# Performance work log

Measured on AMD Instinct MI355X. Metric: run time of the kernel, lower is better.

Reference implementation:

```python
import jax, jax.numpy as jnp
import numpy as np

N = 200000   # nodes
E = 600000   # edges
D = 128      # input_channels
H = 128      # hidden_channels
EPS = 1e-5   # BatchNorm1d eps


def setup_inputs() -> dict:
    key = jax.random.key(0)
    ks = jax.random.split(key, 6)
    x = jax.random.normal(ks[0], (N, D), dtype=jnp.float32)
    edge_index = jax.random.randint(ks[1], (2, E), 0, N)
    a1 = jnp.full((1,), 0.25, dtype=jnp.float32)   # PReLU init
    gamma = jnp.ones((D,), dtype=jnp.float32)
    beta = jnp.zeros((D,), dtype=jnp.float32)
    W1 = jax.random.normal(ks[2], (D, H), dtype=jnp.float32) / np.float32(np.sqrt(D))
    b1 = jnp.zeros((H,), dtype=jnp.float32)
    a2 = jnp.full((1,), 0.25, dtype=jnp.float32)
    W2 = jax.random.normal(ks[3], (H, D), dtype=jnp.float32) / np.float32(np.sqrt(H))
    b2 = jnp.zeros((D,), dtype=jnp.float32)
    return dict(x=x, edge_index=edge_index, a1=a1, gamma=gamma, beta=beta,
                W1=W1, b1=b1, a2=a2, W2=W2, b2=b2)


def _prelu(x, a):
    return jnp.where(x >= 0, x, a[0] * x)


def _batchnorm(x, gamma, beta):
    # training-mode BatchNorm1d: batch mean, biased variance
    mean = jnp.mean(x, axis=0)
    var = jnp.mean(jnp.square(x - mean), axis=0)
    return (x - mean) * jax.lax.rsqrt(var + EPS) * gamma + beta


def _gcn_conv(x, W, b, src, dst, n):
    # PyG GCNConv: add self-loops, symmetric normalization D^-1/2 (A+I) D^-1/2
    h = x @ W                                            # [n, out]
    deg = jnp.ones((n,), h.dtype).at[dst].add(1.0)       # degree incl. self-loop
    dinv = jax.lax.rsqrt(deg)
    coef = (dinv[src] * dinv[dst])[:, None]              # [E, 1]
    msg = h[src] * coef                                  # gather  [E, out]
    out = jax.ops.segment_sum(msg, dst, num_segments=n)  # scatter [n, out]
    out = out + h * (1.0 / deg)[:, None]                 # self-loop term
    return out + b


def reference(x, edge_index, a1, gamma, beta, W1, b1, a2, W2, b2):
    src, dst = edge_index[0], edge_index[1]
    n = x.shape[0]
    h = _prelu(x, a1)
    h = _batchnorm(h, gamma, beta)
    h = _gcn_conv(h, W1, b1, src, dst, n)
    h = _prelu(h, a2)
    h = _gcn_conv(h, W2, b2, src, dst, n)
    return h
```

## Files before the change

### kernel.cpp

```cpp
#include <hip/hip_runtime.h>

#define NN 200000
#define NE 600000
#define DD 128
#define GT 1563

constexpr float BN_EPS = 1e-5f;

typedef unsigned short u16;
typedef short bf16x8 __attribute__((ext_vector_type(8)));
typedef float f32x4  __attribute__((ext_vector_type(4)));


__global__ void k_zero(int* __restrict__ cnt, float* __restrict__ ssum, float* __restrict__ ssq) {
  int i = blockIdx.x*256 + threadIdx.x;
  if (i < NN) cnt[i] = 0;
  if (i < DD) { ssum[i] = 0.f; ssq[i] = 0.f; }
}

__global__ void k_count(const int* __restrict__ ei, int* __restrict__ cnt) {
  int e = blockIdx.x*256 + threadIdx.x;
  if (e < NE) atomicAdd(&cnt[ei[NE + e]], 1);
}

__global__ void k_stats(const float* __restrict__ x, const float* __restrict__ a1p,
                        float* __restrict__ ssum, float* __restrict__ ssq) {
  __shared__ float s1[8][128], s2[8][128];
  const int c4 = (threadIdx.x & 31) * 4;
  const int rg = threadIdx.x >> 5;
  float a1 = *a1p;
  float acc1[4] = {0.f,0.f,0.f,0.f}, acc2[4] = {0.f,0.f,0.f,0.f};
  const int stride = gridDim.x * 8;
  for (int r = blockIdx.x*8 + rg; r < NN; r += stride) {
    float4 v = *(const float4*)(x + (size_t)r*DD + c4);
    float vv[4] = {v.x, v.y, v.z, v.w};
    #pragma unroll
    for (int i = 0; i < 4; ++i) {
      float u = vv[i];
      u = (u >= 0.f) ? u : a1*u;
      acc1[i] += u; acc2[i] += u*u;
    }
  }
  *(float4*)&s1[rg][c4] = make_float4(acc1[0], acc1[1], acc1[2], acc1[3]);
  *(float4*)&s2[rg][c4] = make_float4(acc2[0], acc2[1], acc2[2], acc2[3]);
  __syncthreads();
  if (threadIdx.x < 128) {
    int col = threadIdx.x;
    float t1 = 0.f, t2 = 0.f;
    #pragma unroll
    for (int g = 0; g < 8; ++g) { t1 += s1[g][col]; t2 += s2[g][col]; }
    atomicAdd(&ssum[col], t1);
    atomicAdd(&ssq [col], t2);
  }
}

__global__ void k_bn_tw1(const float* __restrict__ ssum, const float* __restrict__ ssq,
                         const float* __restrict__ gamma, const float* __restrict__ beta,
                         const float* __restrict__ W1,
                         float* __restrict__ sarr, float* __restrict__ tarr,
                         float* __restrict__ tw1) {
  __shared__ float ts[128];
  int j = threadIdx.x;
  float mean = ssum[j] * (1.f/NN);
  float var  = ssq[j] * (1.f/NN) - mean*mean;
  float s = gamma[j] * rsqrtf(var + BN_EPS);
  float t = beta[j] - mean*s;
  sarr[j] = s; tarr[j] = t; ts[j] = t;
  __syncthreads();
  float acc = 0.f;
  #pragma unroll 8
  for (int k = 0; k < 128; ++k) acc += ts[k] * W1[k*DD + j];
  tw1[j] = acc;
}

__global__ void k_wprep(const float* __restrict__ W, const float* __restrict__ s,
                        u16* __restrict__ hi, u16* __restrict__ lo) {
  int idx = blockIdx.x*256 + threadIdx.x;
  int j = idx >> 7, k = idx & 127;
  float v = W[(size_t)k*DD + j];
  if (s) v *= s[k];
  unsigned hb = __float_as_uint(v) & 0xffff0000u;
  float r = v - __uint_as_float(hb);
  hi[idx] = (u16)(hb >> 16);
  lo[idx] = (u16)(__float_as_uint(r) >> 16);
}


__global__ void k_scan1(const int* __restrict__ cnt, int* __restrict__ rp, int* __restrict__ bsums) {
  __shared__ int sm[256];
  int tid = threadIdx.x;
  int base = blockIdx.x*1024 + tid*4;
  int4 v = make_int4(0,0,0,0);
  if (base + 3 < NN) v = *(const int4*)(cnt + base);
  else {
    if (base   < NN) v.x = cnt[base];
    if (base+1 < NN) v.y = cnt[base+1];
    if (base+2 < NN) v.z = cnt[base+2];
    if (base+3 < NN) v.w = cnt[base+3];
  }
  int p1 = v.x, p2 = p1 + v.y, p3 = p2 + v.z, tsum = p3 + v.w;
  sm[tid] = tsum; __syncthreads();
  for (int off = 1; off < 256; off <<= 1) {
    int t = (tid >= off) ? sm[tid - off] : 0; __syncthreads();
    sm[tid] += t; __syncthreads();
  }
  int inc = sm[tid];
  int excl = inc - tsum;
  if (base   < NN) rp[base]   = excl;
  if (base+1 < NN) rp[base+1] = excl + p1;
  if (base+2 < NN) rp[base+2] = excl + p2;
  if (base+3 < NN) rp[base+3] = excl + p3;
  if (tid == 255) bsums[blockIdx.x] = inc;
}

__global__ void k_scan2(int* __restrict__ bsums, int nb) {
  __shared__ int sm[256];
  int tid = threadIdx.x;
  int v = (tid < nb) ? bsums[tid] : 0;
  sm[tid] = v; __syncthreads();
  for (int off = 1; off < 256; off <<= 1) {
    int t = (tid >= off) ? sm[tid - off] : 0; __syncthreads();
    sm[tid] += t; __syncthreads();
  }
  if (tid < nb) bsums[tid] = sm[tid] - v;
}

__global__ void k_scan3(int* __restrict__ rp, const int* __restrict__ bsums,
                        int* __restrict__ cur, const int* __restrict__ cnt,
                        float* __restrict__ dinv) {
  int i = blockIdx.x*256 + threadIdx.x;
  if (i < NN) {
    int val = rp[i] + bsums[i >> 10];
    rp[i] = val; cur[i] = val;
    dinv[i] = rsqrtf((float)(cnt[i] + 1));
  }
  if (i == 0) rp[NN] = NE;
}

__global__ void k_fill(const int* __restrict__ ei, const float* __restrict__ dinv,
                       int* __restrict__ cur, int2* __restrict__ pairs) {
  int e = blockIdx.x*256 + threadIdx.x;
  if (e < NE) {
    int s = ei[e], d = ei[NE + e];
    int pos = atomicAdd(&cur[d], 1);
    float cf = dinv[s] * dinv[d];
    pairs[pos] = make_int2(s, __float_as_int(cf));
  }
}


template<bool FUSE, bool ADDROW>
__global__ __launch_bounds__(256)
void k_gemm(const float* __restrict__ A,
            const u16* __restrict__ wt_hi, const u16* __restrict__ wt_lo,
            float* __restrict__ C,
            const float* __restrict__ tw1, const float* __restrict__ a1p)
{
  __shared__ u16 Bh[128][136];
  __shared__ u16 Bl[128][136];
  const int tid = threadIdx.x;

  #pragma unroll
  for (int i = 0; i < 8; ++i) {
    int c = tid + i*256;
    int row = c >> 4, slot = c & 15;
    *(uint4*)&Bh[row][slot*8] = ((const uint4*)wt_hi)[c];
    *(uint4*)&Bl[row][slot*8] = ((const uint4*)wt_lo)[c];
  }

  float a1v = 0.f;
  if constexpr (FUSE) a1v = *a1p;

  const int lane = tid & 63;
  const int wv   = tid >> 6;
  const int lr   = lane & 15;
  const int lk   = lane >> 4;
  const int r0   = blockIdx.x*128 + wv*32;

  f32x4 acc[2][8];
  #pragma unroll
  for (int s = 0; s < 2; ++s)
    #pragma unroll
    for (int j = 0; j < 8; ++j) acc[s][j] = (f32x4){0.f,0.f,0.f,0.f};

  __syncthreads();

  #pragma unroll
  for (int kc = 0; kc < 4; ++kc) {
    bf16x8 ah[2], al[2];
    #pragma unroll
    for (int s = 0; s < 2; ++s) {
      int r = r0 + s*16 + lr; if (r >= NN) r = NN-1;
      const float* ap = A + (size_t)r*DD + kc*32 + lk*8;
      float4 v0 = *(const float4*)ap;
      float4 v1 = *(const float4*)(ap + 4);
      float vv[8] = {v0.x,v0.y,v0.z,v0.w,v1.x,v1.y,v1.z,v1.w};
      #pragma unroll
      for (int e = 0; e < 8; ++e) {
        float v = vv[e];
        if constexpr (FUSE) v = (v >= 0.f) ? v : a1v*v;
        unsigned hb = __float_as_uint(v) & 0xffff0000u;
        float rres = v - __uint_as_float(hb);
        ah[s][e] = (short)(hb >> 16);
        al[s][e] = (short)(__float_as_uint(rres) >> 16);
      }
    }
    #pragma unroll
    for (int j = 0; j < 8; ++j) {
      int wrow = j*16 + lr;
      bf16x8 bh = *(const bf16x8*)&Bh[wrow][kc*32 + lk*8];
      bf16x8 bl = *(const bf16x8*)&Bl[wrow][kc*32 + lk*8];
      #pragma unroll
      for (int s = 0; s < 2; ++s) {
        acc[s][j] = __builtin_amdgcn_mfma_f32_16x16x32_bf16(ah[s], bh, acc[s][j], 0, 0, 0);
        acc[s][j] = __builtin_amdgcn_mfma_f32_16x16x32_bf16(ah[s], bl, acc[s][j], 0, 0, 0);
        acc[s][j] = __builtin_amdgcn_mfma_f32_16x16x32_bf16(al[s], bh, acc[s][j], 0, 0, 0);
      }
    }
  }

  float tw[8];
  #pragma unroll
  for (int j = 0; j < 8; ++j) tw[j] = 0.f;
  if constexpr (ADDROW) {
    #pragma unroll
    for (int j = 0; j < 8; ++j) tw[j] = tw1[j*16 + lr];
  }

  #pragma unroll
  for (int s = 0; s < 2; ++s) {
    #pragma unroll
    for (int g = 0; g < 4; ++g) {
      int row = r0 + s*16 + lk*4 + g;
      if (row < NN) {
        float* cp = C + (size_t)row*DD + lr;
        #pragma unroll
        for (int j = 0; j < 8; ++j) cp[j*16] = acc[s][j][g] + tw[j];
      }
    }
  }
}


template<bool PRELU>
__global__ __launch_bounds__(256)
void k_agg(const float* __restrict__ h, const int* __restrict__ rp,
           const int2* __restrict__ pairs,
           const float* __restrict__ bias, const float* __restrict__ a2p,
           float* __restrict__ out)
{
  const int wave = threadIdx.x >> 6;
  const int lane = threadIdx.x & 63;
  const int nb = (blockIdx.x*4 + wave) * 8;
  if (nb >= NN) return;
  const float2* h2 = (const float2*)h;
  float2* o2 = (float2*)out;

  int rv = 0;
  if (lane < 9) rv = rp[nb + lane];
  int beg[8], cnt8[8];
  #pragma unroll
  for (int i = 0; i < 8; ++i) {
    int b0 = __builtin_amdgcn_readfirstlane(__shfl(rv, i));
    int b1 = __builtin_amdgcn_readfirstlane(__shfl(rv, i+1));
    beg[i] = b0; cnt8[i] = b1 - b0;
  }

  float2 b = ((const float2*)bias)[lane];
  float a2 = 1.f;
  if constexpr (PRELU) a2 = *a2p;

  float2 acc[8];
  #pragma unroll
  for (int i = 0; i < 8; ++i) {
    float2 self = h2[(size_t)(nb+i)*64 + lane];
    float sc = 1.f / (float)(cnt8[i] + 1);
    acc[i].x = sc*self.x + b.x;
    acc[i].y = sc*self.y + b.y;
  }

  int maxc = 0;
  #pragma unroll
  for (int i = 0; i < 8; ++i) maxc = max(maxc, cnt8[i]);

  for (int c = 0; c < maxc; ++c) {
    int2 p[8];
    #pragma unroll
    for (int i = 0; i < 8; ++i)
      if (c < cnt8[i]) p[i] = pairs[beg[i] + c];
    #pragma unroll
    for (int i = 0; i < 8; ++i)
      if (c < cnt8[i]) {
        float2 g = h2[(size_t)p[i].x*64 + lane];
        float cf = __int_as_float(p[i].y);
        acc[i].x += cf*g.x; acc[i].y += cf*g.y;
      }
  }

  #pragma unroll
  for (int i = 0; i < 8; ++i) {
    float ax = acc[i].x, ay = acc[i].y;
    if constexpr (PRELU) {
      ax = (ax >= 0.f) ? ax : a2*ax;
      ay = (ay >= 0.f) ? ay : a2*ay;
    }
    o2[(size_t)(nb+i)*64 + lane] = make_float2(ax, ay);
  }
}


extern "C" void kernel_launch(void* const* d_in, const int* in_sizes, int n_in,
                              void* d_out, int out_size, void* d_ws, size_t ws_size,
                              hipStream_t stream) {
  const float* x     = (const float*)d_in[0];
  const int*   ei    = (const int*)  d_in[1];
  const float* a1    = (const float*)d_in[2];
  const float* gamma = (const float*)d_in[3];
  const float* beta  = (const float*)d_in[4];
  const float* W1    = (const float*)d_in[5];
  const float* b1    = (const float*)d_in[6];
  const float* a2    = (const float*)d_in[7];
  const float* W2    = (const float*)d_in[8];
  const float* b2    = (const float*)d_in[9];
  float* out = (float*)d_out;

  char* w = (char*)d_ws;
  auto alloc = [&](size_t bytes) { char* p = w; w += (bytes + 255) & ~(size_t)255; return p; };
  float* hbuf  = (float*)alloc((size_t)NN*DD*4);
  float* dinv  = (float*)alloc((size_t)NN*4);
  int*   cnt   = (int*)  alloc((size_t)NN*4);
  int*   rp    = (int*)  alloc((size_t)(NN+1)*4);
  int*   cur   = (int*)  alloc((size_t)NN*4);
  int2*  pairs = (int2*) alloc((size_t)NE*8);
  int*   bsums = (int*)  alloc(256*4);
  float* ssum  = (float*)alloc(128*4);
  float* ssq   = (float*)alloc(128*4);
  float* sarr  = (float*)alloc(128*4);
  float* tarr  = (float*)alloc(128*4);
  float* tw1   = (float*)alloc(128*4);
  u16*   w1h   = (u16*)  alloc(128*128*2);
  u16*   w1l   = (u16*)  alloc(128*128*2);
  u16*   w2h   = (u16*)  alloc(128*128*2);
  u16*   w2l   = (u16*)  alloc(128*128*2);

  const int nblkN = (NN + 255)/256;
  const int nblkE = (NE + 255)/256;
  const int nblkA = NN/32;

  k_zero  <<<nblkN, 256, 0, stream>>>(cnt, ssum, ssq);
  k_count <<<nblkE, 256, 0, stream>>>(ei, cnt);
  k_stats <<<1024,  256, 0, stream>>>(x, a1, ssum, ssq);
  k_bn_tw1<<<1,     128, 0, stream>>>(ssum, ssq, gamma, beta, W1, sarr, tarr, tw1);
  k_wprep <<<64,    256, 0, stream>>>(W2, nullptr, w2h, w2l);
  k_wprep <<<64,    256, 0, stream>>>(W1, sarr,    w1h, w1l);
  k_scan1 <<<196,   256, 0, stream>>>(cnt, rp, bsums);
  k_scan2 <<<1,     256, 0, stream>>>(bsums, 196);
  k_scan3 <<<nblkN, 256, 0, stream>>>(rp, bsums, cur, cnt, dinv);
  k_fill  <<<nblkE, 256, 0, stream>>>(ei, dinv, cur, pairs);

  k_gemm<true,  true ><<<GT, 256, 0, stream>>>(x,   w1h, w1l, hbuf, tw1, a1);
  k_agg <true >        <<<nblkA, 256, 0, stream>>>(hbuf, rp, pairs, b1, a2, out);
  k_gemm<false, false><<<GT, 256, 0, stream>>>(out, w2h, w2l, hbuf, nullptr, nullptr);
  k_agg <false>        <<<nblkA, 256, 0, stream>>>(hbuf, rp, pairs, b2, nullptr, out);
}
```

Before: 511.1 us.

## Fuse first-layer aggregation with second-layer MFMA GEMM into one kernel

Adds k_aggmm, in which each wave aggregates 16 nodes' neighbour features in registers, applies bias and PReLU, splits the result into bf16 hi/lo, and multiplies by W2 with MFMA. This removes the intermediate write and re-read of the aggregated activations and one kernel launch. It needs an extra workspace buffer, with a fallback to the old path when the workspace is too small. The fused gather uses one lane-group per node with a per-wave max-degree loop, so unbalanced degrees can cause divergence, and W2 is read from global memory rather than LDS. The final aggregation's output store is also made nontemporal.

```diff
diff --git a/kernel.cpp b/kernel.cpp
--- a/kernel.cpp
+++ b/kernel.cpp
@@ -10,6 +10,7 @@
 typedef unsigned short u16;
 typedef short bf16x8 __attribute__((ext_vector_type(8)));
 typedef float f32x4  __attribute__((ext_vector_type(4)));
+typedef float f32x2  __attribute__((ext_vector_type(2)));
 
 
 __global__ void k_zero(int* __restrict__ cnt, float* __restrict__ ssum, float* __restrict__ ssq) {
@@ -190,7 +191,7 @@
     bf16x8 ah[2], al[2];
     #pragma unroll
     for (int s = 0; s < 2; ++s) {
-      int r = r0 + s*16 + lr; if (r >= NN) r = NN-1;
+      int r = r0 + s*16 + lr; r = (r < NN) ? r : (NN-1);
       const float* ap = A + (size_t)r*DD + kc*32 + lk*8;
       float4 v0 = *(const float4*)ap;
       float4 v1 = *(const float4*)(ap + 4);
@@ -242,6 +243,101 @@
 }
 
 
+__global__ __launch_bounds__(256)
+void k_aggmm(const float* __restrict__ h, const int* __restrict__ rp,
+             const int2* __restrict__ pairs,
+             const u16* __restrict__ wt_hi, const u16* __restrict__ wt_lo,
+             const float* __restrict__ b1, const float* __restrict__ a2p,
+             float* __restrict__ A2)
+{
+  const int lane = threadIdx.x & 63;
+  const int wave = threadIdx.x >> 6;
+  const int nb   = (blockIdx.x*4 + wave) * 16;
+  const int nd   = lane & 15;
+  const int q    = lane >> 4;
+  const int node = nb + nd;
+
+  int rv = 0;
+  if (lane < 17) rv = rp[nb + lane];
+  int beg = __shfl(rv, nd);
+  int cnt = __shfl(rv, nd + 1) - beg;
+
+  int mc = cnt;
+  #pragma unroll
+  for (int off = 1; off < 16; off <<= 1)
+    mc = max(mc, __shfl_xor(mc, off));
+
+  float acc[4][8];
+  {
+    float sc = 1.f / (float)(cnt + 1);
+    const float* hp = h + (size_t)node*DD + q*8;
+    const float* bp = b1 + q*8;
+    #pragma unroll
+    for (int kc = 0; kc < 4; ++kc) {
+      float4 s0 = *(const float4*)(hp + kc*32);
+      float4 s1 = *(const float4*)(hp + kc*32 + 4);
+      float4 w0 = *(const float4*)(bp + kc*32);
+      float4 w1 = *(const float4*)(bp + kc*32 + 4);
+      acc[kc][0] = sc*s0.x + w0.x; acc[kc][1] = sc*s0.y + w0.y;
+      acc[kc][2] = sc*s0.z + w0.z; acc[kc][3] = sc*s0.w + w0.w;
+      acc[kc][4] = sc*s1.x + w1.x; acc[kc][5] = sc*s1.y + w1.y;
+      acc[kc][6] = sc*s1.z + w1.z; acc[kc][7] = sc*s1.w + w1.w;
+    }
+  }
+
+  const int2* pb = pairs + beg;
+  for (int c = 0; c < mc; ++c) {
+    if (c < cnt) {
+      int2 p = pb[c];
+      float cf = __int_as_float(p.y);
+      const float* gp = h + (size_t)p.x*DD + q*8;
+      #pragma unroll
+      for (int kc = 0; kc < 4; ++kc) {
+        float4 g0 = *(const float4*)(gp + kc*32);
+        float4 g1 = *(const float4*)(gp + kc*32 + 4);
+        acc[kc][0] += cf*g0.x; acc[kc][1] += cf*g0.y;
+        acc[kc][2] += cf*g0.z; acc[kc][3] += cf*g0.w;
+        acc[kc][4] += cf*g1.x; acc[kc][5] += cf*g1.y;
+        acc[kc][6] += cf*g1.z; acc[kc][7] += cf*g1.w;
+      }
+    }
+  }
+
+  float a2 = *a2p;
+  bf16x8 bh[4], bl[4];
+  #pragma unroll
+  for (int kc = 0; kc < 4; ++kc)
+    #pragma unroll
+    for (int e = 0; e < 8; ++e) {
+      float v = acc[kc][e];
+      v = (v >= 0.f) ? v : a2*v;
+      unsigned hb = __float_as_uint(v) & 0xffff0000u;
+      float r = v - __uint_as_float(hb);
+      bh[kc][e] = (short)(hb >> 16);
+      bl[kc][e] = (short)(__float_as_uint(r) >> 16);
+    }
+
+  float* op = A2 + (size_t)node*DD + q*4;
+  const u16* whB = wt_hi + (size_t)nd*DD + q*8;
+  const u16* wlB = wt_lo + (size_t)nd*DD + q*8;
+  #pragma unroll
+  for (int jt = 0; jt < 8; ++jt) {
+    f32x4 d = (f32x4){0.f,0.f,0.f,0.f};
+    const u16* wh = whB + (size_t)jt*16*DD;
+    const u16* wl = wlB + (size_t)jt*16*DD;
+    #pragma unroll
+    for (int kc = 0; kc < 4; ++kc) {
+      bf16x8 ah = *(const bf16x8*)(wh + kc*32);
+      bf16x8 al = *(const bf16x8*)(wl + kc*32);
+      d = __builtin_amdgcn_mfma_f32_16x16x32_bf16(ah, bh[kc], d, 0, 0, 0);
+      d = __builtin_amdgcn_mfma_f32_16x16x32_bf16(ah, bl[kc], d, 0, 0, 0);
+      d = __builtin_amdgcn_mfma_f32_16x16x32_bf16(al, bh[kc], d, 0, 0, 0);
+    }
+    *(float4*)(op + jt*16) = make_float4(d[0], d[1], d[2], d[3]);
+  }
+}
+
+
 template<bool PRELU>
 __global__ __launch_bounds__(256)
 void k_agg(const float* __restrict__ h, const int* __restrict__ rp,
@@ -254,7 +350,7 @@
   const int nb = (blockIdx.x*4 + wave) * 8;
   if (nb >= NN) return;
   const float2* h2 = (const float2*)h;
-  float2* o2 = (float2*)out;
+  f32x2* o2 = (f32x2*)out;
 
   int rv = 0;
   if (lane < 9) rv = rp[nb + lane];
@@ -304,7 +400,8 @@
       ax = (ax >= 0.f) ? ax : a2*ax;
       ay = (ay >= 0.f) ? ay : a2*ay;
     }
-    o2[(size_t)(nb+i)*64 + lane] = make_float2(ax, ay);
+    f32x2 o; o[0] = ax; o[1] = ay;
+    __builtin_nontemporal_store(o, &o2[(size_t)(nb+i)*64 + lane]);
   }
 }
 
@@ -342,10 +439,13 @@
   u16*   w1l   = (u16*)  alloc(128*128*2);
   u16*   w2h   = (u16*)  alloc(128*128*2);
   u16*   w2l   = (u16*)  alloc(128*128*2);
+  float* hbuf2 = (float*)alloc((size_t)NN*DD*4);
+  const bool fused = ((size_t)(w - (char*)d_ws) <= ws_size);
 
   const int nblkN = (NN + 255)/256;
   const int nblkE = (NE + 255)/256;
   const int nblkA = NN/32;
+  const int nblkF = NN/64;
 
   k_zero  <<<nblkN, 256, 0, stream>>>(cnt, ssum, ssq);
   k_count <<<nblkE, 256, 0, stream>>>(ei, cnt);
@@ -358,8 +458,13 @@
   k_scan3 <<<nblkN, 256, 0, stream>>>(rp, bsums, cur, cnt, dinv);
   k_fill  <<<nblkE, 256, 0, stream>>>(ei, dinv, cur, pairs);
 
-  k_gemm<true,  true ><<<GT, 256, 0, stream>>>(x,   w1h, w1l, hbuf, tw1, a1);
-  k_agg <true >        <<<nblkA, 256, 0, stream>>>(hbuf, rp, pairs, b1, a2, out);
-  k_gemm<false, false><<<GT, 256, 0, stream>>>(out, w2h, w2l, hbuf, nullptr, nullptr);
-  k_agg <false>        <<<nblkA, 256, 0, stream>>>(hbuf, rp, pairs, b2, nullptr, out);
-}
+  k_gemm<true, true><<<GT, 256, 0, stream>>>(x, w1h, w1l, hbuf, tw1, a1);
+  if (fused) {
+    k_aggmm<<<nblkF, 256, 0, stream>>>(hbuf, rp, pairs, w2h, w2l, b1, a2, hbuf2);
+    k_agg<false><<<nblkA, 256, 0, stream>>>(hbuf2, rp, pairs, b2, nullptr, out);
+  } else {
+    k_agg<true >         <<<nblkA, 256, 0, stream>>>(hbuf, rp, pairs, b1, a2, out);
+    k_gemm<false, false><<<GT, 256, 0, stream>>>(out, w2h, w2l, hbuf, nullptr, nullptr);
+    k_agg<false>         <<<nblkA, 256, 0, stream>>>(hbuf, rp, pairs, b2, nullptr, out);
+  }
+}
```

After: 554.5 us. 1.09x slower.
